# Kernel optimization log

Measured on AMD Instinct MI355X. Metric: run time of the kernel, lower is better.

The kernel has to match this reference:

```python
import jax, jax.numpy as jnp
import numpy as np

N, T_PLUS_1, D_IN, WV, HID, V = 64, 33, 1024, 512, 1024, 32000
NULL_IDX = 0


def setup_inputs() -> dict:
    key = jax.random.key(0)
    ks = jax.random.split(key, 9)
    return {
        "features": jax.random.normal(ks[0], (N, D_IN, 4, 4), jnp.float32),
        "captions": jax.random.randint(ks[1], (N, T_PLUS_1), 0, V),
        "W_embed": jax.random.normal(ks[2], (V, WV), jnp.float32) / np.float32(np.sqrt(V)),
        "Wx": jax.random.normal(ks[3], (WV, 4 * HID), jnp.float32) / np.float32(np.sqrt(WV)),
        "Wh": jax.random.normal(ks[4], (HID, 4 * HID), jnp.float32) / np.float32(np.sqrt(HID)),
        "Wattn": jax.random.normal(ks[5], (HID, 4 * HID), jnp.float32) / np.float32(np.sqrt(HID)),
        "b": jnp.zeros((4 * HID,), jnp.float32),
        "W_proj": jax.random.normal(ks[6], (D_IN, HID), jnp.float32) / np.float32(np.sqrt(D_IN)),
        "b_proj": jnp.zeros((HID,), jnp.float32),
        "W_out": jax.random.normal(ks[7], (HID, V), jnp.float32) / np.float32(np.sqrt(HID)),
        "b_out": jnp.zeros((V,), jnp.float32),
    }


def reference(features, captions, W_embed, Wx, Wh, Wattn, b, W_proj, b_proj, W_out, b_out):
    n, _ = captions.shape
    cap_in = captions[:, :-1]   # [N, T]
    cap_out = captions[:, 1:]   # [N, T]

    # project_input applied channel-last: A is [N, H, 4, 4]
    A = jnp.einsum('ndhw,dk->nkhw', features, W_proj) + b_proj[None, :, None, None]
    h0 = A.mean(axis=(2, 3))  # [N, H]
    c0 = h0
    hdim = h0.shape[1]
    A_flat = A.reshape(n, hdim, -1)  # [N, H, P] with P = 16 grid cells
    inv_sqrt_h = jnp.float32(1.0 / np.sqrt(hdim))

    x = W_embed[cap_in]  # [N, T, WV]

    def step(carry, x_t):
        prev_h, prev_c = carry
        # dot-product attention over the spatial grid
        s = jnp.einsum('nh,nhp->np', prev_h, A_flat) * inv_sqrt_h
        w = jax.nn.softmax(s, axis=-1)
        attn = jnp.einsum('nhp,np->nh', A_flat, w)
        # LSTM gating
        a = x_t @ Wx + prev_h @ Wh + attn @ Wattn + b
        i = jax.nn.sigmoid(a[:, :hdim])
        f = jax.nn.sigmoid(a[:, hdim:2 * hdim])
        o = jax.nn.sigmoid(a[:, 2 * hdim:3 * hdim])
        g = jnp.tanh(a[:, 3 * hdim:])
        next_c = f * prev_c + i * g
        next_h = o * jnp.tanh(next_c)
        return (next_h, next_c), next_h

    _, hs = jax.lax.scan(step, (h0, c0), x.transpose(1, 0, 2))  # hs: [T, N, H]
    h = hs.transpose(1, 0, 2)  # [N, T, H]

    scores = h @ W_out + b_out  # [N, T, V]
    logp = jax.nn.log_softmax(scores, axis=-1)
    nll = -jnp.take_along_axis(logp, cap_out[..., None], axis=-1)[..., 0]  # [N, T]
    mask = (cap_out != NULL_IDX).astype(nll.dtype)
    loss = jnp.sum(nll * mask) / n
    return loss
```

## Files before the change

### kernel.cpp

```cpp
#include <hip/hip_runtime.h>
#include <hip/hip_bf16.h>
#include <math.h>

typedef __attribute__((ext_vector_type(8))) short short8;
typedef __attribute__((ext_vector_type(4))) float f32x4;
typedef unsigned short ushort_t;
typedef unsigned int uint_t;

typedef __attribute__((address_space(1))) const void gvoid_t;
typedef __attribute__((address_space(3))) void lvoid_t;

#define VTILES 250

static __device__ __forceinline__ ushort_t f2b(float f){
  __hip_bfloat16 h = __float2bfloat16(f);
  return *reinterpret_cast<ushort_t*>(&h);
}
static __device__ __forceinline__ float b2f(ushort_t u){
  __hip_bfloat16 h = *reinterpret_cast<__hip_bfloat16*>(&u);
  return __bfloat162float(h);
}
static __device__ __forceinline__ float sigmoidf_(float x){ return 1.0f/(1.0f+__expf(-x)); }

__global__ void k_transpose_cvt(const float* __restrict__ src, ushort_t* __restrict__ dst,
                                int C, int dstride, int dcoloff) {
  __shared__ ushort_t tile[64][72];
  int cb = blockIdx.x * 64, rb = blockIdx.y * 64;
  int tid = threadIdx.x;
  for (int it = 0; it < 4; ++it) {
    int e = tid + it*256;
    int row = e >> 4;
    int seg = e & 15;
    float4 v = *reinterpret_cast<const float4*>(&src[(size_t)(rb+row)*C + cb + seg*4]);
    tile[seg*4+0][row] = f2b(v.x);
    tile[seg*4+1][row] = f2b(v.y);
    tile[seg*4+2][row] = f2b(v.z);
    tile[seg*4+3][row] = f2b(v.w);
  }
  __syncthreads();
  for (int it = 0; it < 2; ++it) {
    int e = tid + it*256;
    int cl = e >> 3;
    int seg = e & 7;
    uint4 v = *reinterpret_cast<uint4*>(&tile[cl][seg*8]);
    *reinterpret_cast<uint4*>(&dst[(size_t)(cb+cl)*dstride + dcoloff + rb + seg*8]) = v;
  }
}

__global__ void k_featT(const float* __restrict__ feat, ushort_t* __restrict__ fBT) {
  __shared__ ushort_t t[16][264];
  int n = blockIdx.x;
  int tid = threadIdx.x;
  for (int it = 0; it < 4; ++it) {
    int d = it*256 + tid;
    const float* src = &feat[((size_t)n*1024 + d)*16];
    #pragma unroll
    for (int q = 0; q < 4; ++q) {
      float4 v = *reinterpret_cast<const float4*>(&src[q*4]);
      t[q*4+0][tid] = f2b(v.x);
      t[q*4+1][tid] = f2b(v.y);
      t[q*4+2][tid] = f2b(v.z);
      t[q*4+3][tid] = f2b(v.w);
    }
    __syncthreads();
    #pragma unroll
    for (int w = 0; w < 2; ++w) {
      int e = tid + w*256;
      int p = e >> 5;
      int seg = e & 31;
      uint4 v = *reinterpret_cast<uint4*>(&t[p][seg*8]);
      *reinterpret_cast<uint4*>(&fBT[((size_t)n*16 + p)*1024 + it*256 + seg*8]) = v;
    }
    __syncthreads();
  }
}

__global__ void k_embed(const int* __restrict__ captions, const float* __restrict__ W_embed,
                        ushort_t* __restrict__ xb) {
  int e = (blockIdx.x*256 + threadIdx.x) * 4;
  int nt = e >> 9;
  int n = nt >> 5, t = nt & 31;
  int col = e & 511;
  int tok = captions[n*33 + t];
  float4 v = *reinterpret_cast<const float4*>(&W_embed[(size_t)tok*512 + col]);
  ushort4 o; o.x=f2b(v.x); o.y=f2b(v.y); o.z=f2b(v.z); o.w=f2b(v.w);
  *reinterpret_cast<ushort4*>(&xb[e]) = o;
}

__global__ void k_projmm(const ushort_t* __restrict__ WprojT, const ushort_t* __restrict__ fBT,
                         const float* __restrict__ b_proj, float* __restrict__ A_flat,
                         ushort_t* __restrict__ Abt) {
  __shared__ ushort_t As[64*64];
  __shared__ ushort_t Bs[64*64];
  int kt = blockIdx.x, nt = blockIdx.y;
  int k0 = kt*64, n0 = nt*64;
  int tid = threadIdx.x;
  int wave = tid>>6, lane = tid&63, lr = lane&15, lg = lane>>4;
  int srow = lane>>3, sxor8 = ((lane&7)^srow)*8;
  f32x4 acc[4];
  #pragma unroll
  for (int nf=0;nf<4;++nf) acc[nf] = (f32x4){0.f,0.f,0.f,0.f};
  for (int kc = 0; kc < 1024; kc += 64){
    __syncthreads();
    #pragma unroll
    for (int u = 0; u < 2; ++u){
      int r0 = wave*16 + u*8;
      const ushort_t* srcA = &WprojT[(size_t)(k0 + r0 + srow)*1024 + kc + sxor8];
      const ushort_t* srcB = &fBT[(size_t)(n0 + r0 + srow)*1024 + kc + sxor8];
      __builtin_amdgcn_global_load_lds((gvoid_t*)srcA, (lvoid_t*)&As[r0*64], 16, 0, 0);
      __builtin_amdgcn_global_load_lds((gvoid_t*)srcB, (lvoid_t*)&Bs[r0*64], 16, 0, 0);
    }
    __syncthreads();
    #pragma unroll
    for (int kk = 0; kk < 2; ++kk){
      int swz = (((kk*4 + lg) ^ (lr & 7)) * 8);
      short8 af = *reinterpret_cast<short8*>(&As[(wave*16 + lr)*64 + swz]);
      #pragma unroll
      for (int nf = 0; nf < 4; ++nf){
        short8 bf = *reinterpret_cast<short8*>(&Bs[(nf*16 + lr)*64 + swz]);
        acc[nf] = __builtin_amdgcn_mfma_f32_16x16x32_bf16(af, bf, acc[nf], 0, 0, 0);
      }
    }
  }
  #pragma unroll
  for (int nf=0;nf<4;++nf){
    int ncol = n0 + nf*16 + lr;
    int nidx = ncol >> 4, p = ncol & 15;
    ushort4 ab;
    #pragma unroll
    for (int r=0;r<4;++r){
      int kh = k0 + wave*16 + lg*4 + r;
      float val = acc[nf][r] + b_proj[kh];
      A_flat[((size_t)nidx*1024 + kh)*16 + p] = val;
      (&ab.x)[r] = f2b(val);
    }
    *reinterpret_cast<ushort4*>(&Abt[(size_t)ncol*1024 + k0 + wave*16 + lg*4]) = ab;
  }
}

__global__ void k_h0(const float* __restrict__ A_flat, float* __restrict__ hbuf) {
  int idx = blockIdx.x*256 + threadIdx.x;
  const float* a = &A_flat[(size_t)idx*16];
  float s = 0.f;
  #pragma unroll
  for (int p=0;p<16;p+=4){
    float4 v = *reinterpret_cast<const float4*>(&a[p]);
    s += v.x+v.y+v.z+v.w;
  }
  hbuf[idx] = s * (1.f/16.f);
}

__global__ void k_pmm(const ushort_t* __restrict__ WcatT, const ushort_t* __restrict__ Abt,
                      ushort_t* __restrict__ P2) {
  __shared__ ushort_t As[64*64];
  __shared__ ushort_t Bs[64*64];
  __shared__ ushort_t Dt2[64][72];
  int jt = blockIdx.x, nt = blockIdx.y;
  int j0 = jt*64, n0 = nt*64;
  int tid = threadIdx.x;
  int wave = tid>>6, lane = tid&63, lr = lane&15, lg = lane>>4;
  int srow = lane>>3, sxor8 = ((lane&7)^srow)*8;
  f32x4 acc[4];
  #pragma unroll
  for (int nf=0;nf<4;++nf) acc[nf] = (f32x4){0.f,0.f,0.f,0.f};
  for (int kc = 0; kc < 1024; kc += 64){
    __syncthreads();
    #pragma unroll
    for (int u = 0; u < 2; ++u){
      int r0 = wave*16 + u*8;
      const ushort_t* srcA = &WcatT[(size_t)(j0 + r0 + srow)*2560 + 1536 + kc + sxor8];
      const ushort_t* srcB = &Abt[(size_t)(n0 + r0 + srow)*1024 + kc + sxor8];
      __builtin_amdgcn_global_load_lds((gvoid_t*)srcA, (lvoid_t*)&As[r0*64], 16, 0, 0);
      __builtin_amdgcn_global_load_lds((gvoid_t*)srcB, (lvoid_t*)&Bs[r0*64], 16, 0, 0);
    }
    __syncthreads();
    #pragma unroll
    for (int kk = 0; kk < 2; ++kk){
      int swz = (((kk*4 + lg) ^ (lr & 7)) * 8);
      short8 af = *reinterpret_cast<short8*>(&As[(wave*16 + lr)*64 + swz]);
      #pragma unroll
      for (int nf = 0; nf < 4; ++nf){
        short8 bf = *reinterpret_cast<short8*>(&Bs[(nf*16 + lr)*64 + swz]);
        acc[nf] = __builtin_amdgcn_mfma_f32_16x16x32_bf16(af, bf, acc[nf], 0, 0, 0);
      }
    }
  }
  __syncthreads();
  #pragma unroll
  for (int nf=0;nf<4;++nf)
    #pragma unroll
    for (int r=0;r<4;++r)
      Dt2[wave*16 + lg*4 + r][nf*16 + lr] = f2b(acc[nf][r]);
  __syncthreads();
  #pragma unroll
  for (int it=0; it<2; ++it){
    int e = it*256 + tid;
    int row = e >> 3, seg = e & 7;
    uint4 v = *reinterpret_cast<uint4*>(&Dt2[row][seg*8]);
    *reinterpret_cast<uint4*>(&P2[(size_t)(j0+row)*1024 + n0 + seg*8]) = v;
  }
}

__global__ void k_xmm(const ushort_t* __restrict__ WcatT, const ushort_t* __restrict__ xb,
                      ushort_t* __restrict__ xpre) {
  __shared__ ushort_t As[64*64];
  __shared__ ushort_t Bs[64*64];
  __shared__ float Dt[64][68];
  int jt = blockIdx.x, mt = blockIdx.y;
  int j0 = jt*64, m0 = mt*64;
  int tid = threadIdx.x;
  int wave = tid>>6, lane = tid&63, lr = lane&15, lg = lane>>4;
  int srow = lane>>3, sxor8 = ((lane&7)^srow)*8;
  f32x4 acc[4];
  #pragma unroll
  for (int nf=0;nf<4;++nf) acc[nf] = (f32x4){0.f,0.f,0.f,0.f};
  for (int kc = 0; kc < 512; kc += 64){
    __syncthreads();
    #pragma unroll
    for (int u = 0; u < 2; ++u){
      int r0 = wave*16 + u*8;
      const ushort_t* srcA = &WcatT[(size_t)(j0 + r0 + srow)*2560 + kc + sxor8];
      const ushort_t* srcB = &xb[(size_t)(m0 + r0 + srow)*512 + kc + sxor8];
      __builtin_amdgcn_global_load_lds((gvoid_t*)srcA, (lvoid_t*)&As[r0*64], 16, 0, 0);
      __builtin_amdgcn_global_load_lds((gvoid_t*)srcB, (lvoid_t*)&Bs[r0*64], 16, 0, 0);
    }
    __syncthreads();
    #pragma unroll
    for (int kk = 0; kk < 2; ++kk){
      int swz = (((kk*4 + lg) ^ (lr & 7)) * 8);
      short8 af = *reinterpret_cast<short8*>(&As[(wave*16 + lr)*64 + swz]);
      #pragma unroll
      for (int nf = 0; nf < 4; ++nf){
        short8 bf = *reinterpret_cast<short8*>(&Bs[(nf*16 + lr)*64 + swz]);
        acc[nf] = __builtin_amdgcn_mfma_f32_16x16x32_bf16(af, bf, acc[nf], 0, 0, 0);
      }
    }
  }
  __syncthreads();
  #pragma unroll
  for (int nf=0; nf<4; ++nf)
    #pragma unroll
    for (int r=0;r<4;++r)
      Dt[nf*16+lr][wave*16 + lg*4 + r] = acc[nf][r];
  __syncthreads();
  #pragma unroll
  for (int it=0; it<4; ++it){
    int e = tid + it*256;
    int nrow = e >> 4, seg = e & 15;
    float4 v = *reinterpret_cast<float4*>(&Dt[nrow][seg*4]);
    ushort4 o; o.x=f2b(v.x); o.y=f2b(v.y); o.z=f2b(v.z); o.w=f2b(v.w);
    *reinterpret_cast<ushort4*>(&xpre[(size_t)(m0+nrow)*4096 + j0 + seg*4]) = o;
  }
}

__global__ void k_gate(int i, const ushort_t* __restrict__ xpre, const float* __restrict__ a_part,
                       const float* __restrict__ bvec, const ushort_t* __restrict__ P2,
                       const float* __restrict__ A_flat, const float* __restrict__ hbuf,
                       float* __restrict__ cbuf, const float* __restrict__ sp_rd,
                       float* __restrict__ sp_wr, ushort_t* __restrict__ hbf,
                       ushort_t* __restrict__ hall) {
  __shared__ float wvLds[16];
  __shared__ float wred[4][16];
  int n = blockIdx.x >> 2, sp = blockIdx.x & 3;
  int tid = threadIdx.x;
  int wave = tid>>6, lane = tid&63;
  int k = sp*256 + tid;
  float hv;
  if (i == 0){
    hv = hbuf[n*1024 + k];
    cbuf[n*1024 + k] = hv;
    hbf[n*1024 + k] = f2b(hv);
  } else {
    if (tid < 16){
      float sv = (sp_rd[(n*4+0)*16+tid] + sp_rd[(n*4+1)*16+tid] +
                  sp_rd[(n*4+2)*16+tid] + sp_rd[(n*4+3)*16+tid]) * (1.f/32.f);
      float m = sv;
      #pragma unroll
      for (int d=1; d<16; d<<=1) m = fmaxf(m, __shfl_xor(m, d, 64));
      float e = __expf(sv - m);
      float s = e;
      #pragma unroll
      for (int d=1; d<16; d<<=1) s += __shfl_xor(s, d, 64);
      wvLds[tid] = e / s;
    }
    __syncthreads();
    float wv[16];
    #pragma unroll
    for (int p=0;p<16;++p) wv[p] = wvLds[p];
    float av[4];
    #pragma unroll
    for (int g=0;g<4;++g){
      int j = g*1024 + k;
      float x = bvec[j] + b2f(xpre[(size_t)(n*32 + (i-1))*4096 + j]);
      #pragma unroll
      for (int ks=0;ks<4;++ks) x += a_part[((size_t)ks*64 + n)*4096 + j];
      const ushort_t* pp = &P2[(size_t)j*1024 + (n<<4)];
      short8 p0 = *reinterpret_cast<const short8*>(pp);
      short8 p1 = *reinterpret_cast<const short8*>(pp+8);
      #pragma unroll
      for (int p=0;p<8;++p) x += wv[p]*b2f((ushort_t)p0[p]);
      #pragma unroll
      for (int p=0;p<8;++p) x += wv[8+p]*b2f((ushort_t)p1[p]);
      av[g]=x;
    }
    float ig=sigmoidf_(av[0]), fg=sigmoidf_(av[1]), og=sigmoidf_(av[2]), gg=tanhf(av[3]);
    float c = fg*cbuf[n*1024+k] + ig*gg;
    hv = og*tanhf(c);
    cbuf[n*1024+k] = c;
    hall[((size_t)n*32 + (i-1))*1024 + k] = f2b(hv);
    if (i < 32) hbf[n*1024+k] = f2b(hv);
  }
  if (i == 32) return;
  float sacc[16];
  const float* An = &A_flat[((size_t)n*1024 + k)*16];
  #pragma unroll
  for (int p=0;p<16;p+=4){
    float4 a4 = *reinterpret_cast<const float4*>(&An[p]);
    sacc[p] = hv*a4.x; sacc[p+1] = hv*a4.y; sacc[p+2] = hv*a4.z; sacc[p+3] = hv*a4.w;
  }
  #pragma unroll
  for (int d=1; d<64; d<<=1)
    #pragma unroll
    for (int p=0;p<16;++p) sacc[p] += __shfl_xor(sacc[p], d, 64);
  if (lane == 0)
    #pragma unroll
    for (int p=0;p<16;++p) wred[wave][p] = sacc[p];
  __syncthreads();
  if (tid < 16)
    sp_wr[(n*4+sp)*16 + tid] = wred[0][tid]+wred[1][tid]+wred[2][tid]+wred[3][tid];
}

__global__ void k_mm(const ushort_t* __restrict__ WcatT, const ushort_t* __restrict__ hbf,
                     float* __restrict__ a_part) {
  __shared__ ushort_t As[64*64];
  __shared__ ushort_t Bs[64*64];
  __shared__ float Dt[64][68];
  int jt = blockIdx.x, ks = blockIdx.y;
  int j0 = jt*64;
  int tid = threadIdx.x;
  int wave = tid>>6, lane = tid&63, lr = lane&15, lg = lane>>4;
  int srow = lane>>3, sxor8 = ((lane&7)^srow)*8;
  f32x4 acc[4];
  #pragma unroll
  for (int nf=0;nf<4;++nf) acc[nf] = (f32x4){0.f,0.f,0.f,0.f};
  for (int kc = 0; kc < 256; kc += 64){
    __syncthreads();
    #pragma unroll
    for (int u = 0; u < 2; ++u){
      int r0 = wave*16 + u*8;
      const ushort_t* srcA = &WcatT[(size_t)(j0 + r0 + srow)*2560 + 512 + ks*256 + kc + sxor8];
      const ushort_t* srcB = &hbf[(size_t)(r0 + srow)*1024 + ks*256 + kc + sxor8];
      __builtin_amdgcn_global_load_lds((gvoid_t*)srcA, (lvoid_t*)&As[r0*64], 16, 0, 0);
      __builtin_amdgcn_global_load_lds((gvoid_t*)srcB, (lvoid_t*)&Bs[r0*64], 16, 0, 0);
    }
    __syncthreads();
    #pragma unroll
    for (int kk = 0; kk < 2; ++kk){
      int swz = (((kk*4 + lg) ^ (lr & 7)) * 8);
      short8 af = *reinterpret_cast<short8*>(&As[(wave*16 + lr)*64 + swz]);
      #pragma unroll
      for (int nf = 0; nf < 4; ++nf){
        short8 bf = *reinterpret_cast<short8*>(&Bs[(nf*16 + lr)*64 + swz]);
        acc[nf] = __builtin_amdgcn_mfma_f32_16x16x32_bf16(af, bf, acc[nf], 0, 0, 0);
      }
    }
  }
  __syncthreads();
  #pragma unroll
  for (int nf=0; nf<4; ++nf)
    #pragma unroll
    for (int r=0;r<4;++r)
      Dt[nf*16+lr][wave*16 + lg*4 + r] = acc[nf][r];
  __syncthreads();
  #pragma unroll
  for (int it=0; it<4; ++it){
    int e = tid + it*256;
    int nrow = e >> 4, seg = e & 15;
    float4 v = *reinterpret_cast<float4*>(&Dt[nrow][seg*4]);
    *reinterpret_cast<float4*>(&a_part[((size_t)ks*64 + nrow)*4096 + j0 + seg*4]) = v;
  }
}

__global__ void __launch_bounds__(256, 4)
k_score(const ushort_t* __restrict__ WoutT, const ushort_t* __restrict__ hall,
        const float* __restrict__ b_out,
        float* __restrict__ pmax, float* __restrict__ psum) {
  __shared__ ushort_t As[128*64];
  __shared__ ushort_t Bs[128*64];
  __shared__ float bLds[128];
  __shared__ float pmLds[4][128];
  __shared__ float psLds[4][128];
  int bid = blockIdx.x;
  int wg = (bid & 7) * 500 + (bid >> 3);
  int vb = wg >> 4, rb = wg & 15;
  int v0 = vb * 128, r0 = rb * 128;
  int tid = threadIdx.x;
  int wave = tid >> 6, lane = tid & 63, lr = lane & 15, lg = lane >> 4;
  if (tid < 128) bLds[tid] = b_out[v0 + tid];

  int srow = lane >> 3;
  int sxor = ((lane & 7) ^ srow) << 3;

  f32x4 acc[2][8];
  #pragma unroll
  for (int a=0;a<2;++a)
    #pragma unroll
    for (int q=0;q<8;++q) acc[a][q]=(f32x4){0.f,0.f,0.f,0.f};

  for (int kc = 0; kc < 1024; kc += 64) {
    __syncthreads();
    #pragma unroll
    for (int i = 0; i < 4; ++i) {
      int rowg = (wave*4 + i) * 8;
      const ushort_t* gsA = &WoutT[(size_t)(v0 + rowg + srow)*1024 + kc + sxor];
      const ushort_t* gsB = &hall [(size_t)(r0 + rowg + srow)*1024 + kc + sxor];
      __builtin_amdgcn_global_load_lds((gvoid_t*)gsA, (lvoid_t*)&As[rowg*64], 16, 0, 0);
      __builtin_amdgcn_global_load_lds((gvoid_t*)gsB, (lvoid_t*)&Bs[rowg*64], 16, 0, 0);
    }
    __syncthreads();
    #pragma unroll
    for (int kk = 0; kk < 2; ++kk) {
      int swz = ((kk*4 + lg) ^ (lr & 7)) << 3;
      int rowA = wave*32 + lr;
      short8 af0 = *reinterpret_cast<short8*>(&As[rowA*64 + swz]);
      short8 af1 = *reinterpret_cast<short8*>(&As[(rowA+16)*64 + swz]);
      #pragma unroll
      for (int nr = 0; nr < 8; ++nr) {
        short8 bf = *reinterpret_cast<short8*>(&Bs[(nr*16+lr)*64 + swz]);
        acc[0][nr] = __builtin_amdgcn_mfma_f32_16x16x32_bf16(af0, bf, acc[0][nr], 0,0,0);
        acc[1][nr] = __builtin_amdgcn_mfma_f32_16x16x32_bf16(af1, bf, acc[1][nr], 0,0,0);
      }
    }
  }
  #pragma unroll
  for (int nr=0;nr<8;++nr){
    float m = -1e30f;
    float xv[8];
    #pragma unroll
    for (int mv=0;mv<2;++mv)
      #pragma unroll
      for (int r=0;r<4;++r){
        float x = acc[mv][nr][r] + bLds[wave*32 + mv*16 + lg*4 + r];
        xv[mv*4+r]=x; m = fmaxf(m,x);
      }
    float s=0.f;
    #pragma unroll
    for (int i=0;i<8;++i) s += __expf(xv[i]-m);
    #pragma unroll
    for (int d=16; d<=32; d<<=1){
      float om = __shfl_xor(m, d, 64);
      float os = __shfl_xor(s, d, 64);
      float nm = fmaxf(m, om);
      s = s*__expf(m-nm) + os*__expf(om-nm);
      m = nm;
    }
    if (lg == 0){
      pmLds[wave][nr*16+lr] = m;
      psLds[wave][nr*16+lr] = s;
    }
  }
  __syncthreads();
  if (tid < 128){
    float m=-1e30f;
    #pragma unroll
    for (int w=0;w<4;++w) m = fmaxf(m, pmLds[w][tid]);
    float s=0.f;
    #pragma unroll
    for (int w=0;w<4;++w) s += psLds[w][tid]*__expf(pmLds[w][tid]-m);
    pmax[(size_t)(r0+tid)*VTILES + vb] = m;
    psum[(size_t)(r0+tid)*VTILES + vb] = s;
  }
}

__global__ void k_tgt(const ushort_t* __restrict__ hall, const ushort_t* __restrict__ WoutT,
                      const float* __restrict__ b_out, const int* __restrict__ captions,
                      float* __restrict__ stgt) {
  int tid = threadIdx.x;
  int wave = tid>>6, lane = tid&63;
  int r = blockIdx.x*4 + wave;
  int n = r>>5, t = r&31;
  int y = captions[n*33 + t + 1];
  const ushort_t* hrow = hall + (size_t)r*1024;
  const ushort_t* wrow = WoutT + (size_t)y*1024;
  float dot = 0.f;
  #pragma unroll
  for (int i=0;i<2;++i){
    int off = lane*8 + i*512;
    short8 hv = *reinterpret_cast<const short8*>(&hrow[off]);
    short8 wv = *reinterpret_cast<const short8*>(&wrow[off]);
    #pragma unroll
    for (int e2=0;e2<8;++e2) dot += b2f((ushort_t)hv[e2])*b2f((ushort_t)wv[e2]);
  }
  #pragma unroll
  for (int d=32; d>=1; d>>=1) dot += __shfl_xor(dot, d, 64);
  if (lane==0) stgt[r] = dot + b_out[y];
}

__global__ void k_reduce(const float* __restrict__ pmax, const float* __restrict__ psum,
                         const float* __restrict__ stgt, const int* __restrict__ captions,
                         float* __restrict__ row_loss) {
  int tid = threadIdx.x;
  int wave = tid>>6, lane = tid&63;
  int r = blockIdx.x*4 + wave;
  float m = -1e30f, s = 0.f;
  for (int j = lane; j < VTILES; j += 64){
    float mj = pmax[(size_t)r*VTILES + j];
    float sj = psum[(size_t)r*VTILES + j];
    float nm = fmaxf(m, mj);
    s = s*__expf(m-nm) + sj*__expf(mj-nm);
    m = nm;
  }
  #pragma unroll
  for (int d=32; d>=1; d>>=1){
    float om = __shfl_xor(m, d, 64);
    float os = __shfl_xor(s, d, 64);
    float nm = fmaxf(m, om);
    s = s*__expf(m-nm) + os*__expf(om-nm);
    m = nm;
  }
  if (lane==0){
    int n = r>>5, t = r&31;
    int y = captions[n*33 + t + 1];
    float lse = m + __logf(s);
    row_loss[r] = (y != 0) ? (lse - stgt[r]) : 0.f;
  }
}

__global__ void k_final(const float* __restrict__ row_loss, float* __restrict__ out) {
  __shared__ float red[256];
  int tid = threadIdx.x;
  float s = 0.f;
  #pragma unroll
  for (int i=0;i<8;++i) s += row_loss[tid + i*256];
  red[tid] = s;
  __syncthreads();
  for (int off=128; off>=1; off>>=1){
    if (tid<off) red[tid] += red[tid+off];
    __syncthreads();
  }
  if (tid==0) out[0] = red[0] * (1.f/64.f);
}

extern "C" void kernel_launch(void* const* d_in, const int* in_sizes, int n_in,
                              void* d_out, int out_size, void* d_ws, size_t ws_size,
                              hipStream_t stream) {
  const float* features = (const float*)d_in[0];
  const int*   captions = (const int*)d_in[1];
  const float* W_embed  = (const float*)d_in[2];
  const float* Wx       = (const float*)d_in[3];
  const float* Wh       = (const float*)d_in[4];
  const float* Wattn    = (const float*)d_in[5];
  const float* b        = (const float*)d_in[6];
  const float* W_proj   = (const float*)d_in[7];
  const float* b_proj   = (const float*)d_in[8];
  const float* W_out    = (const float*)d_in[9];
  const float* b_out    = (const float*)d_in[10];
  float* out = (float*)d_out;

  char* wsp = (char*)d_ws;
  size_t off = 0;
  auto alloc = [&](size_t bytes)->char*{
    char* p = wsp + off; off += (bytes + 255) & ~(size_t)255; return p;
  };
  ushort_t* WcatT  = (ushort_t*)alloc((size_t)4096*2560*2);
  ushort_t* WoutT  = (ushort_t*)alloc((size_t)32000*1024*2);
  ushort_t* WprojT = (ushort_t*)alloc((size_t)1024*1024*2);
  ushort_t* fBT    = (ushort_t*)alloc((size_t)1024*1024*2);
  ushort_t* Abt    = (ushort_t*)alloc((size_t)1024*1024*2);
  float* A_flat    = (float*)alloc((size_t)64*1024*16*4);
  ushort_t* xb     = (ushort_t*)alloc((size_t)64*32*512*2);
  float* hbuf      = (float*)alloc((size_t)64*1024*4);
  ushort_t* P2     = (ushort_t*)alloc((size_t)4096*1024*2);
  ushort_t* xpre   = (ushort_t*)alloc((size_t)2048*4096*2);
  float* a_part    = (float*)alloc((size_t)4*64*4096*4);
  ushort_t* hbf    = (ushort_t*)alloc((size_t)64*1024*2);
  float* cbuf      = (float*)alloc((size_t)64*1024*4);
  float* spbuf     = (float*)alloc((size_t)2*64*4*16*4);
  ushort_t* hall   = (ushort_t*)alloc((size_t)2048*1024*2);
  float* pmax      = (float*)alloc((size_t)2048*250*4);
  float* psum      = (float*)alloc((size_t)2048*250*4);
  float* stgt      = (float*)alloc((size_t)2048*4);
  float* row_loss  = (float*)alloc((size_t)2048*4);

  hipLaunchKernelGGL(k_transpose_cvt, dim3(64, 8),   dim3(256), 0, stream, Wx,     WcatT,  4096, 2560, 0);
  hipLaunchKernelGGL(k_transpose_cvt, dim3(64, 16),  dim3(256), 0, stream, Wh,     WcatT,  4096, 2560, 512);
  hipLaunchKernelGGL(k_transpose_cvt, dim3(64, 16),  dim3(256), 0, stream, Wattn,  WcatT,  4096, 2560, 1536);
  hipLaunchKernelGGL(k_transpose_cvt, dim3(500, 16), dim3(256), 0, stream, W_out,  WoutT,  32000, 1024, 0);
  hipLaunchKernelGGL(k_transpose_cvt, dim3(16, 16),  dim3(256), 0, stream, W_proj, WprojT, 1024, 1024, 0);
  hipLaunchKernelGGL(k_featT, dim3(64), dim3(256), 0, stream, features, fBT);
  hipLaunchKernelGGL(k_embed, dim3(1024), dim3(256), 0, stream, captions, W_embed, xb);
  hipLaunchKernelGGL(k_projmm, dim3(16, 16), dim3(256), 0, stream, WprojT, fBT, b_proj, A_flat, Abt);
  hipLaunchKernelGGL(k_h0, dim3(256), dim3(256), 0, stream, A_flat, hbuf);
  hipLaunchKernelGGL(k_pmm, dim3(64, 16), dim3(256), 0, stream, WcatT, Abt, P2);
  hipLaunchKernelGGL(k_xmm, dim3(64, 32), dim3(256), 0, stream, WcatT, xb, xpre);

  for (int i = 0; i <= 32; ++i){
    const float* sp_rd = spbuf + ((i+1)&1)*4096;
    float*       sp_wr = spbuf + (i&1)*4096;
    hipLaunchKernelGGL(k_gate, dim3(256), dim3(256), 0, stream, i, xpre, a_part, b, P2,
                       A_flat, hbuf, cbuf, sp_rd, sp_wr, hbf, hall);
    if (i < 32)
      hipLaunchKernelGGL(k_mm, dim3(64, 4), dim3(256), 0, stream, WcatT, hbf, a_part);
  }

  hipLaunchKernelGGL(k_score, dim3(4000), dim3(256), 0, stream, WoutT, hall, b_out, pmax, psum);
  hipLaunchKernelGGL(k_tgt, dim3(512), dim3(256), 0, stream, hall, WoutT, b_out, captions, stgt);
  hipLaunchKernelGGL(k_reduce, dim3(512), dim3(256), 0, stream, pmax, psum, stgt, captions, row_loss);
  hipLaunchKernelGGL(k_final, dim3(1), dim3(256), 0, stream, row_loss, out);
}
```

Measured before the change: 700.7 us.

## Fuse h0 mean into projection, relayout P for gate reads, split recurrent K 8-way

Result: faster. 673.1 us (-3.9%).

```diff
diff --git a/kernel.cpp b/kernel.cpp
--- a/kernel.cpp
+++ b/kernel.cpp
@@ -89,7 +89,7 @@
 
 __global__ void k_projmm(const ushort_t* __restrict__ WprojT, const ushort_t* __restrict__ fBT,
                          const float* __restrict__ b_proj, float* __restrict__ A_flat,
-                         ushort_t* __restrict__ Abt) {
+                         ushort_t* __restrict__ Abt, float* __restrict__ hbuf) {
   __shared__ ushort_t As[64*64];
   __shared__ ushort_t Bs[64*64];
   int kt = blockIdx.x, nt = blockIdx.y;
@@ -133,25 +133,19 @@
       float val = acc[nf][r] + b_proj[kh];
       A_flat[((size_t)nidx*1024 + kh)*16 + p] = val;
       (&ab.x)[r] = f2b(val);
+      float s = val;
+      s += __shfl_xor(s, 1, 64);
+      s += __shfl_xor(s, 2, 64);
+      s += __shfl_xor(s, 4, 64);
+      s += __shfl_xor(s, 8, 64);
+      if (lr == 0) hbuf[(nt*4 + nf)*1024 + kh] = s * (1.f/16.f);
     }
     *reinterpret_cast<ushort4*>(&Abt[(size_t)ncol*1024 + k0 + wave*16 + lg*4]) = ab;
   }
 }
 
-__global__ void k_h0(const float* __restrict__ A_flat, float* __restrict__ hbuf) {
-  int idx = blockIdx.x*256 + threadIdx.x;
-  const float* a = &A_flat[(size_t)idx*16];
-  float s = 0.f;
-  #pragma unroll
-  for (int p=0;p<16;p+=4){
-    float4 v = *reinterpret_cast<const float4*>(&a[p]);
-    s += v.x+v.y+v.z+v.w;
-  }
-  hbuf[idx] = s * (1.f/16.f);
-}
-
 __global__ void k_pmm(const ushort_t* __restrict__ WcatT, const ushort_t* __restrict__ Abt,
-                      ushort_t* __restrict__ P2) {
+                      ushort_t* __restrict__ P3) {
   __shared__ ushort_t As[64*64];
   __shared__ ushort_t Bs[64*64];
   __shared__ ushort_t Dt2[64][72];
@@ -197,7 +191,7 @@
     int e = it*256 + tid;
     int row = e >> 3, seg = e & 7;
     uint4 v = *reinterpret_cast<uint4*>(&Dt2[row][seg*8]);
-    *reinterpret_cast<uint4*>(&P2[(size_t)(j0+row)*1024 + n0 + seg*8]) = v;
+    *reinterpret_cast<uint4*>(&P3[(((size_t)nt*4 + (seg>>1))*4096 + j0 + row)*16 + (seg&1)*8]) = v;
   }
 }
 
@@ -254,7 +248,7 @@
 }
 
 __global__ void k_gate(int i, const ushort_t* __restrict__ xpre, const float* __restrict__ a_part,
-                       const float* __restrict__ bvec, const ushort_t* __restrict__ P2,
+                       const float* __restrict__ bvec, const ushort_t* __restrict__ P3,
                        const float* __restrict__ A_flat, const float* __restrict__ hbuf,
                        float* __restrict__ cbuf, const float* __restrict__ sp_rd,
                        float* __restrict__ sp_wr, ushort_t* __restrict__ hbf,
@@ -293,8 +287,8 @@
       int j = g*1024 + k;
       float x = bvec[j] + b2f(xpre[(size_t)(n*32 + (i-1))*4096 + j]);
       #pragma unroll
-      for (int ks=0;ks<4;++ks) x += a_part[((size_t)ks*64 + n)*4096 + j];
-      const ushort_t* pp = &P2[(size_t)j*1024 + (n<<4)];
+      for (int ks=0;ks<8;++ks) x += a_part[((size_t)ks*64 + n)*4096 + j];
+      const ushort_t* pp = &P3[((size_t)n*4096 + j)*16];
       short8 p0 = *reinterpret_cast<const short8*>(pp);
       short8 p1 = *reinterpret_cast<const short8*>(pp+8);
       #pragma unroll
@@ -343,13 +337,13 @@
   f32x4 acc[4];
   #pragma unroll
   for (int nf=0;nf<4;++nf) acc[nf] = (f32x4){0.f,0.f,0.f,0.f};
-  for (int kc = 0; kc < 256; kc += 64){
+  for (int kc = 0; kc < 128; kc += 64){
     __syncthreads();
     #pragma unroll
     for (int u = 0; u < 2; ++u){
       int r0 = wave*16 + u*8;
-      const ushort_t* srcA = &WcatT[(size_t)(j0 + r0 + srow)*2560 + 512 + ks*256 + kc + sxor8];
-      const ushort_t* srcB = &hbf[(size_t)(r0 + srow)*1024 + ks*256 + kc + sxor8];
+      const ushort_t* srcA = &WcatT[(size_t)(j0 + r0 + srow)*2560 + 512 + ks*128 + kc + sxor8];
+      const ushort_t* srcB = &hbf[(size_t)(r0 + srow)*1024 + ks*128 + kc + sxor8];
       __builtin_amdgcn_global_load_lds((gvoid_t*)srcA, (lvoid_t*)&As[r0*64], 16, 0, 0);
       __builtin_amdgcn_global_load_lds((gvoid_t*)srcB, (lvoid_t*)&Bs[r0*64], 16, 0, 0);
     }
@@ -570,9 +564,9 @@
   float* A_flat    = (float*)alloc((size_t)64*1024*16*4);
   ushort_t* xb     = (ushort_t*)alloc((size_t)64*32*512*2);
   float* hbuf      = (float*)alloc((size_t)64*1024*4);
-  ushort_t* P2     = (ushort_t*)alloc((size_t)4096*1024*2);
+  ushort_t* P3     = (ushort_t*)alloc((size_t)64*4096*16*2);
   ushort_t* xpre   = (ushort_t*)alloc((size_t)2048*4096*2);
-  float* a_part    = (float*)alloc((size_t)4*64*4096*4);
+  float* a_part    = (float*)alloc((size_t)8*64*4096*4);
   ushort_t* hbf    = (ushort_t*)alloc((size_t)64*1024*2);
   float* cbuf      = (float*)alloc((size_t)64*1024*4);
   float* spbuf     = (float*)alloc((size_t)2*64*4*16*4);
@@ -589,18 +583,17 @@
   hipLaunchKernelGGL(k_transpose_cvt, dim3(16, 16),  dim3(256), 0, stream, W_proj, WprojT, 1024, 1024, 0);
   hipLaunchKernelGGL(k_featT, dim3(64), dim3(256), 0, stream, features, fBT);
   hipLaunchKernelGGL(k_embed, dim3(1024), dim3(256), 0, stream, captions, W_embed, xb);
-  hipLaunchKernelGGL(k_projmm, dim3(16, 16), dim3(256), 0, stream, WprojT, fBT, b_proj, A_flat, Abt);
-  hipLaunchKernelGGL(k_h0, dim3(256), dim3(256), 0, stream, A_flat, hbuf);
-  hipLaunchKernelGGL(k_pmm, dim3(64, 16), dim3(256), 0, stream, WcatT, Abt, P2);
+  hipLaunchKernelGGL(k_projmm, dim3(16, 16), dim3(256), 0, stream, WprojT, fBT, b_proj, A_flat, Abt, hbuf);
+  hipLaunchKernelGGL(k_pmm, dim3(64, 16), dim3(256), 0, stream, WcatT, Abt, P3);
   hipLaunchKernelGGL(k_xmm, dim3(64, 32), dim3(256), 0, stream, WcatT, xb, xpre);
 
   for (int i = 0; i <= 32; ++i){
     const float* sp_rd = spbuf + ((i+1)&1)*4096;
     float*       sp_wr = spbuf + (i&1)*4096;
-    hipLaunchKernelGGL(k_gate, dim3(256), dim3(256), 0, stream, i, xpre, a_part, b, P2,
+    hipLaunchKernelGGL(k_gate, dim3(256), dim3(256), 0, stream, i, xpre, a_part, b, P3,
                        A_flat, hbuf, cbuf, sp_rd, sp_wr, hbf, hall);
     if (i < 32)
-      hipLaunchKernelGGL(k_mm, dim3(64, 4), dim3(256), 0, stream, WcatT, hbf, a_part);
+      hipLaunchKernelGGL(k_mm, dim3(64, 8), dim3(256), 0, stream, WcatT, hbf, a_part);
   }
 
   hipLaunchKernelGGL(k_score, dim3(4000), dim3(256), 0, stream, WoutT, hall, b_out, pmax, psum);
```
